# Performance work log

Hardware: AMD Instinct MI355X
Metric: run time of the kernel (lower is better)

## Reference

```python
import jax, jax.numpy as jnp
import numpy as np

N0, N1, N2 = 100000, 25000, 6250
F = 128
OUT = 5


def _mean_agg(feat_src, src, dst, n_dst):
    # DGL copy_u + mean: segment mean over destination nodes (0 for isolated dst)
    s = jax.ops.segment_sum(feat_src[src], dst, num_segments=n_dst)
    cnt = jax.ops.segment_sum(jnp.ones_like(dst, dtype=feat_src.dtype), dst, num_segments=n_dst)
    return s / jnp.maximum(cnt, 1.0)[:, None]


def _graph_conv(feat, src, dst, W, b, n):
    # DGL GraphConv, norm='both': D_src^-1/2 gather-sum D_dst^-1/2, then linear
    dt = feat.dtype
    out_deg = jax.ops.segment_sum(jnp.ones_like(src, dtype=dt), src, num_segments=n)
    in_deg = jax.ops.segment_sum(jnp.ones_like(dst, dtype=dt), dst, num_segments=n)
    ns = jnp.where(out_deg > 0, out_deg ** -0.5, 0.0)
    nd = jnp.where(in_deg > 0, in_deg ** -0.5, 0.0)
    agg = jax.ops.segment_sum((feat * ns[:, None])[src], dst, num_segments=n)
    return (agg * nd[:, None]) @ W + b


def setup_inputs() -> dict:
    key = jax.random.key(0)
    keys = jax.random.split(key, 64)
    _c = iter(range(64))
    def nrm(shape, s=0.05):
        return jax.random.normal(keys[next(_c)], shape, dtype=jnp.float32) * s
    def ri(n, hi):
        return jax.random.randint(keys[next(_c)], (n,), 0, hi)
    inp = {
        'X': nrm((N0, 32), 1.0),
        'g0_src': ri(1600000, N0), 'g0_dst': ri(1600000, N0),
        'g1_src': ri(400000, N1), 'g1_dst': ri(400000, N1),
        'g2_src': ri(100000, N2), 'g2_dst': ri(100000, N2),
        'inc0_src': ri(100000, N0), 'inc0_dst': ri(100000, N1),
        'inc1_src': ri(25000, N1), 'inc1_dst': ri(25000, N2),
        'dec0_src': ri(100000, N2), 'dec0_dst': ri(100000, N1),
        'dec1_src': ri(400000, N1), 'dec1_dst': ri(400000, N0),
        'W_emb': nrm((32, F)), 'b_emb': jnp.zeros((F,), jnp.float32),
        'W_gcn0': nrm((F, F)), 'b_gcn0': jnp.zeros((F,), jnp.float32),
        'W_gcn1': nrm((F, F)), 'b_gcn1': jnp.zeros((F,), jnp.float32),
        'W_gcn2': nrm((F, F)), 'b_gcn2': jnp.zeros((F,), jnp.float32),
        'W_enc0': nrm((F, F)), 'b_enc0': jnp.zeros((F,), jnp.float32),
        'W_enc1': nrm((F, F)), 'b_enc1': jnp.zeros((F,), jnp.float32),
        'W_dec0': nrm((F, F)), 'b_dec0': jnp.zeros((F,), jnp.float32),
        'W_dec1': nrm((F, F)), 'b_dec1': jnp.zeros((F,), jnp.float32),
        'W_head0': nrm((2 * F, OUT)), 'b_head0': jnp.zeros((OUT,), jnp.float32),
        'W_head1': nrm((2 * F, OUT)), 'b_head1': jnp.zeros((OUT,), jnp.float32),
        'W_head2': nrm((2 * F, OUT)), 'b_head2': jnp.zeros((OUT,), jnp.float32),
    }
    return inp


def reference(X, g0_src, g0_dst, g1_src, g1_dst, g2_src, g2_dst,
              inc0_src, inc0_dst, inc1_src, inc1_dst,
              dec0_src, dec0_dst, dec1_src, dec1_dst,
              W_emb, b_emb, W_gcn0, b_gcn0, W_gcn1, b_gcn1, W_gcn2, b_gcn2,
              W_enc0, b_enc0, W_enc1, b_enc1, W_dec0, b_dec0, W_dec1, b_dec1,
              W_head0, b_head0, W_head1, b_head1, W_head2, b_head2):
    # embedding at finest scale
    h0 = X @ W_emb + b_emb                                   # [N0, F]
    # encode + pool fine -> coarse (copy_u/mean)
    h1 = _mean_agg(h0 @ W_enc0 + b_enc0, inc0_src, inc0_dst, N1)   # [N1, F]
    h2 = _mean_agg(h1 @ W_enc1 + b_enc1, inc1_src, inc1_dst, N2)   # [N2, F]
    # intra-scale GraphConv
    g0 = _graph_conv(h0, g0_src, g0_dst, W_gcn0, b_gcn0, N0)
    g1 = _graph_conv(h1, g1_src, g1_dst, W_gcn1, b_gcn1, N1)
    g2 = _graph_conv(h2, g2_src, g2_dst, W_gcn2, b_gcn2, N2)
    # decode coarse -> fine
    d2 = g2
    d1 = _mean_agg(d2 @ W_dec0 + b_dec0, dec0_src, dec0_dst, N1)   # [N1, F]
    d0 = _mean_agg(d1 @ W_dec1 + b_dec1, dec1_src, dec1_dst, N0)   # [N0, F]
    # per-scale heads with softmax
    o0 = jax.nn.softmax(jnp.concatenate([g0, d0], -1) @ W_head0 + b_head0, axis=-1)
    o1 = jax.nn.softmax(jnp.concatenate([g1, d1], -1) @ W_head1 + b_head1, axis=-1)
    o2 = jax.nn.softmax(jnp.concatenate([g2, d2], -1) @ W_head2 + b_head2, axis=-1)
    return jnp.concatenate([o0, o1, o2], axis=0)             # [N0+N1+N2, OUT]
```

## Files before the change

### kernel.cpp

```cpp
#include <hip/hip_runtime.h>

#define F 128
static const int N0 = 100000, N1 = 25000, N2 = 6250;

typedef unsigned short u16;
typedef unsigned int   u32;
typedef __attribute__((ext_vector_type(8))) short bf16x8;
typedef __attribute__((ext_vector_type(4))) float f32x4;

__device__ __forceinline__ float bf2f(u16 u) {
    union { u32 i; float f; } v; v.i = ((u32)u) << 16; return v.f;
}
__device__ __forceinline__ u16 f2bf(float f) {
    u32 u = __float_as_uint(f);
    u += 0x7fff + ((u >> 16) & 1);
    return (u16)(u >> 16);
}

struct Seg7 {
    const int* src[7];
    const int* dst[7];
    int end[7];
    int cbase[7];
    int obase[7];
};

#define EPT 4
#define SM32  (64*(32+8)*2 + 128*(32+8)*2 + 128*4)
#define SM128 (64*(128+8)*2 + 128*(128+8)*2 + 128*4)


template <int K, bool AF32, bool MASK>
__device__ __forceinline__ void dev_mm(char* smem, const void* __restrict__ Ap,
                                       const float* __restrict__ W,
                                       const float* __restrict__ bias,
                                       u16* __restrict__ out,
                                       const int* __restrict__ rowptr,
                                       int M, int blk) {
    const int AST = K + 8;
    const int WST = K + 8;
    u16* Al = (u16*)smem;
    u16* Wt = (u16*)(smem + 64 * AST * 2);
    float* bl = (float*)(smem + 64 * AST * 2 + 128 * WST * 2);
    int tid = threadIdx.x;
    int m0 = blk * 64;

    for (int i = tid; i < K * 128; i += 256) {
        int k = i >> 7, n = i & 127;
        Wt[n * WST + k] = f2bf(W[i]);
    }
    for (int i = tid; i < 64 * K; i += 256) {
        int r = i / K, c = i % K;
        int gr = m0 + r;
        u16 v = 0;
        if (gr < M) {
            if (AF32) v = f2bf(((const float*)Ap)[(size_t)gr * K + c]);
            else      v = ((const u16*)Ap)[(size_t)gr * K + c];
        }
        Al[r * AST + c] = v;
    }
    if (tid < 128) bl[tid] = bias[tid];
    __syncthreads();

    int w = tid >> 6;
    int lane = tid & 63;
    int m16 = lane & 15;
    int quad = lane >> 4;

    f32x4 acc[8];
#pragma unroll
    for (int t = 0; t < 8; t++)
#pragma unroll
        for (int r = 0; r < 4; r++) acc[t][r] = 0.f;

    for (int k0 = 0; k0 < K; k0 += 32) {
        bf16x8 af = *(const bf16x8*)&Al[(w * 16 + m16) * AST + k0 + quad * 8];
#pragma unroll
        for (int t = 0; t < 8; t++) {
            bf16x8 bf = *(const bf16x8*)&Wt[(t * 16 + m16) * WST + k0 + quad * 8];
            acc[t] = __builtin_amdgcn_mfma_f32_16x16x32_bf16(af, bf, acc[t], 0, 0, 0);
        }
    }

#pragma unroll
    for (int t = 0; t < 8; t++) {
#pragma unroll
        for (int r = 0; r < 4; r++) {
            int gr = m0 + w * 16 + quad * 4 + r;
            if (gr >= M) continue;
            int gc = t * 16 + m16;
            bool zrow = false;
            if (MASK) zrow = (rowptr[gr + 1] == rowptr[gr]);
            float v = acc[t][r] + bl[gc];
            out[(size_t)gr * F + gc] = zrow ? (u16)0 : f2bf(v);
        }
    }
}

template <int MODE>
__device__ __forceinline__ void dev_gather(const u16* __restrict__ feat,
                                           const int* __restrict__ rowptr,
                                           const int* __restrict__ col,
                                           const float* __restrict__ odr,
                                           u16* __restrict__ out, int M, int blk) {
    int wv = (blk * 256 + (int)threadIdx.x) >> 6;
    if (wv >= M) return;
    int lane = threadIdx.x & 63;
    int fo = lane << 1;
    int beg = rowptr[wv], end = rowptr[wv + 1];
    float a0 = 0.f, a1 = 0.f;
    int j = beg;
    for (; j + 8 <= end; j += 8) {
        int cc[8];
#pragma unroll
        for (int t = 0; t < 8; t++) cc[t] = col[j + t];
        float ss[8];
#pragma unroll
        for (int t = 0; t < 8; t++) ss[t] = (MODE == 1) ? odr[cc[t]] : 1.f;
        ushort2 uu[8];
#pragma unroll
        for (int t = 0; t < 8; t++) uu[t] = *(const ushort2*)&feat[(size_t)cc[t] * F + fo];
#pragma unroll
        for (int t = 0; t < 8; t++) { a0 += bf2f(uu[t].x) * ss[t]; a1 += bf2f(uu[t].y) * ss[t]; }
    }
    for (; j < end; j++) {
        int c = col[j];
        float s = (MODE == 1) ? odr[c] : 1.f;
        ushort2 u = *(const ushort2*)&feat[(size_t)c * F + fo];
        a0 += bf2f(u.x) * s; a1 += bf2f(u.y) * s;
    }
    int deg = end - beg;
    float fs = (MODE == 0) ? (deg > 0 ? 1.f / (float)deg : 0.f)
                           : (deg > 0 ? rsqrtf((float)deg) : 0.f);
    ushort2 o; o.x = f2bf(a0 * fs); o.y = f2bf(a1 * fs);
    *(ushort2*)&out[(size_t)wv * F + fo] = o;
}

__device__ __forceinline__ void dev_head(char* smem, const u16* __restrict__ g,
                                         const u16* __restrict__ d,
                                         const float* __restrict__ Wh,
                                         const float* __restrict__ bh,
                                         float* __restrict__ out, int M, int blk) {
    float* Wl = (float*)smem;
    float* bl = (float*)(smem + 1280 * 4);
    int tid = threadIdx.x;
    for (int i = tid; i < 1280; i += 256) Wl[i] = Wh[i];
    if (tid < 5) bl[tid] = bh[tid];
    __syncthreads();

    int lane = tid & 63;
    int wv = tid >> 6;
    int r0 = blk * 32 + wv * 8;
    int k0 = lane << 1;
    for (int i = 0; i < 8; i++) {
        int row = r0 + i;
        if (row < M) {
            ushort2 gu = *(const ushort2*)&g[(size_t)row * F + k0];
            ushort2 du = *(const ushort2*)&d[(size_t)row * F + k0];
            float g0v = bf2f(gu.x), g1v = bf2f(gu.y);
            float d0v = bf2f(du.x), d1v = bf2f(du.y);
            float p[5];
#pragma unroll
            for (int o = 0; o < 5; o++) {
                p[o] = g0v * Wl[k0 * 5 + o] + g1v * Wl[(k0 + 1) * 5 + o] +
                       d0v * Wl[(k0 + 128) * 5 + o] + d1v * Wl[(k0 + 129) * 5 + o];
            }
#pragma unroll
            for (int o = 0; o < 5; o++) {
                float v = p[o];
                v += __shfl_xor(v, 32, 64);
                v += __shfl_xor(v, 16, 64);
                v += __shfl_xor(v, 8, 64);
                v += __shfl_xor(v, 4, 64);
                v += __shfl_xor(v, 2, 64);
                v += __shfl_xor(v, 1, 64);
                p[o] = v + bl[o];
            }
            if (lane == 0) {
                float m = p[0];
#pragma unroll
                for (int o = 1; o < 5; o++) m = fmaxf(m, p[o]);
                float e[5], s = 0.f;
#pragma unroll
                for (int o = 0; o < 5; o++) { e[o] = expf(p[o] - m); s += e[o]; }
                float inv = 1.f / s;
#pragma unroll
                for (int o = 0; o < 5; o++) out[(size_t)row * 5 + o] = e[o] * inv;
            }
        }
    }
}


__global__ __launch_bounds__(256) void k_count_emb(Seg7 S, int* __restrict__ cnt,
                                                   int* __restrict__ od,
                                                   u16* __restrict__ occ, int ETOT,
                                                   const float* __restrict__ X,
                                                   const float* __restrict__ Wemb,
                                                   const float* __restrict__ bemb,
                                                   u16* __restrict__ h0, int nbMM) {
    __shared__ char smem[SM32];
    if ((int)blockIdx.x < nbMM) {
        dev_mm<32, true, false>(smem, X, Wemb, bemb, h0, nullptr, N0, blockIdx.x);
        return;
    }
    int e = ((int)blockIdx.x - nbMM) * 256 + threadIdx.x;
    if (e >= ETOT) return;
    int s = 0;
    while (e >= S.end[s]) s++;
    int le = e - ((s == 0) ? 0 : S.end[s - 1]);
    occ[e] = (u16)atomicAdd(&cnt[S.cbase[s] + S.dst[s][le]], 1);
    int ob = S.obase[s];
    if (ob >= 0) atomicAdd(&od[ob + S.src[s][le]], 1);
}

__global__ __launch_bounds__(256) void k_fill_odr(Seg7 S,
                                                  const int* __restrict__ rowptr,
                                                  const u16* __restrict__ occ,
                                                  int* __restrict__ col, int ETOT,
                                                  float invRow, int nbFill,
                                                  const int* __restrict__ od,
                                                  float* __restrict__ odr, int nod) {
    if ((int)blockIdx.x >= nbFill) {
        int i = ((int)blockIdx.x - nbFill) * 256 + threadIdx.x;
        if (i < nod) { int o = od[i]; odr[i] = o > 0 ? rsqrtf((float)o) : 0.f; }
        return;
    }
    int win = blockIdx.x & 7;
    int base = ((int)blockIdx.x >> 3) * (256 * EPT) + threadIdx.x;
#pragma unroll
    for (int t = 0; t < EPT; t++) {
        int e = base + t * 256;
        if (e >= ETOT) break;
        int s = 0;
        while (e >= S.end[s]) s++;
        int le = e - ((s == 0) ? 0 : S.end[s - 1]);
        int grow = S.cbase[s] + S.dst[s][le];
        int w1 = (int)((float)grow * invRow); w1 = w1 > 7 ? 7 : w1;
        if (w1 == win) {
            col[rowptr[grow] + (int)occ[e]] = S.src[s][le];
        }
    }
}

#define SCHUNK 4096
__global__ __launch_bounds__(1024) void k_scan1(const int* __restrict__ cnt,
                                                int* __restrict__ partial, int n) {
    __shared__ int red[1024];
    int tid = threadIdx.x;
    int base = blockIdx.x * SCHUNK + tid * 4;
    int s = 0;
#pragma unroll
    for (int j = 0; j < 4; j++) { int i = base + j; if (i < n) s += cnt[i]; }
    red[tid] = s;
    __syncthreads();
    for (int d = 512; d > 0; d >>= 1) {
        if (tid < d) red[tid] += red[tid + d];
        __syncthreads();
    }
    if (tid == 0) partial[blockIdx.x] = red[0];
}

__global__ __launch_bounds__(128) void k_scan2(int* __restrict__ partial, int G) {
    __shared__ int sh[128];
    int tid = threadIdx.x;
    sh[tid] = (tid < G) ? partial[tid] : 0;
    __syncthreads();
    for (int d = 1; d < 128; d <<= 1) {
        int t = (tid >= d) ? sh[tid - d] : 0;
        __syncthreads();
        sh[tid] += t;
        __syncthreads();
    }
    if (tid < G) partial[tid] = (tid > 0) ? sh[tid - 1] : 0;
    if (tid == 127) partial[G] = sh[127];
}

__global__ __launch_bounds__(1024) void k_scan3(const int* __restrict__ cnt,
                                                const int* __restrict__ partial,
                                                int* __restrict__ rowptr,
                                                int n, int G) {
    __shared__ int red[1024];
    int tid = threadIdx.x;
    int base = blockIdx.x * SCHUNK + tid * 4;
    int v0 = 0, v1 = 0, v2 = 0, v3 = 0;
    if (base + 0 < n) v0 = cnt[base + 0];
    if (base + 1 < n) v1 = cnt[base + 1];
    if (base + 2 < n) v2 = cnt[base + 2];
    if (base + 3 < n) v3 = cnt[base + 3];
    red[tid] = v0 + v1 + v2 + v3;
    __syncthreads();
    for (int d = 1; d < 1024; d <<= 1) {
        int t = (tid >= d) ? red[tid - d] : 0;
        __syncthreads();
        red[tid] += t;
        __syncthreads();
    }
    int off = partial[blockIdx.x] + ((tid > 0) ? red[tid - 1] : 0);
    if (base + 0 < n) { rowptr[base + 0] = off; off += v0; }
    if (base + 1 < n) { rowptr[base + 1] = off; off += v1; }
    if (base + 2 < n) { rowptr[base + 2] = off; off += v2; }
    if (base + 3 < n) { rowptr[base + 3] = off; off += v3; }
    if (blockIdx.x == 0 && tid == 0) rowptr[n] = partial[G];
}

template <int MODE>
__global__ __launch_bounds__(256) void k_gather(const u16* __restrict__ feat,
                                                const int* __restrict__ rowptr,
                                                const int* __restrict__ col,
                                                const float* __restrict__ odr,
                                                u16* __restrict__ out, int M) {
    dev_gather<MODE>(feat, rowptr, col, odr, out, M, blockIdx.x);
}

template <int K, bool AF32, bool MASK>
__global__ __launch_bounds__(256) void k_mm(const void* __restrict__ Ap,
                                            const float* __restrict__ W,
                                            const float* __restrict__ bias,
                                            u16* __restrict__ out,
                                            const int* __restrict__ rowptr,
                                            int M) {
    __shared__ char smem[K == 32 ? SM32 : SM128];
    dev_mm<K, AF32, MASK>(smem, Ap, W, bias, out, rowptr, M, blockIdx.x);
}

template <int MA, int MB>
__global__ __launch_bounds__(256) void k_gather2(
    const u16* fA, const int* rpA, const float* oA, u16* outA, int MAr, int nbA,
    const u16* fB, const int* rpB, const float* oB, u16* outB, int MBr,
    const int* __restrict__ col) {
    if ((int)blockIdx.x < nbA) dev_gather<MA>(fA, rpA, col, oA, outA, MAr, blockIdx.x);
    else                       dev_gather<MB>(fB, rpB, col, oB, outB, MBr, blockIdx.x - nbA);
}

__global__ __launch_bounds__(256) void k_mm2(
    const u16* A1, const float* W1, const float* b1, u16* o1, const int* rp1, int M1, int nb1,
    const u16* A2, const float* W2, const float* b2, u16* o2, int M2) {
    __shared__ char smem[SM128];
    if ((int)blockIdx.x < nb1) dev_mm<128, false, true >(smem, A1, W1, b1, o1, rp1, M1, blockIdx.x);
    else                       dev_mm<128, false, false>(smem, A2, W2, b2, o2, nullptr, M2, blockIdx.x - nb1);
}

__global__ __launch_bounds__(256) void k_head3(
    const u16* Ga, const u16* Da, const float* Wa, const float* Ba, int nb0,
    const u16* Gb, const u16* Db, const float* Wb, const float* Bb, int nb1,
    const u16* Gc, const float* Wc, const float* Bc,
    float* __restrict__ out) {
    __shared__ char smem[1280 * 4 + 32];
    int b = blockIdx.x;
    if (b < nb0)            dev_head(smem, Ga, Da, Wa, Ba, out, N0, b);
    else if (b < nb0 + nb1) dev_head(smem, Gb, Db, Wb, Bb, out + (size_t)N0 * 5, N1, b - nb0);
    else                    dev_head(smem, Gc, Gc, Wc, Bc, out + (size_t)(N0 + N1) * 5, N2, b - nb0 - nb1);
}

extern "C" void kernel_launch(void* const* d_in, const int* in_sizes, int n_in,
                              void* d_out, int out_size, void* d_ws, size_t ws_size,
                              hipStream_t stream) {
    const float* X = (const float*)d_in[0];
    const int *g0s = (const int*)d_in[1], *g0d = (const int*)d_in[2];
    const int *g1s = (const int*)d_in[3], *g1d = (const int*)d_in[4];
    const int *g2s = (const int*)d_in[5], *g2d = (const int*)d_in[6];
    const int *i0s = (const int*)d_in[7], *i0d = (const int*)d_in[8];
    const int *i1s = (const int*)d_in[9], *i1d = (const int*)d_in[10];
    const int *dc0s = (const int*)d_in[11], *dc0d = (const int*)d_in[12];
    const int *dc1s = (const int*)d_in[13], *dc1d = (const int*)d_in[14];
    const float *Wemb = (const float*)d_in[15], *bemb = (const float*)d_in[16];
    const float *Wg0 = (const float*)d_in[17], *bg0 = (const float*)d_in[18];
    const float *Wg1 = (const float*)d_in[19], *bg1 = (const float*)d_in[20];
    const float *Wg2 = (const float*)d_in[21], *bg2 = (const float*)d_in[22];
    const float *We0 = (const float*)d_in[23], *be0 = (const float*)d_in[24];
    const float *We1 = (const float*)d_in[25], *be1 = (const float*)d_in[26];
    const float *Wd0 = (const float*)d_in[27], *bd0 = (const float*)d_in[28];
    const float *Wd1 = (const float*)d_in[29], *bd1 = (const float*)d_in[30];
    const float *Wh0 = (const float*)d_in[31], *bh0 = (const float*)d_in[32];
    const float *Wh1 = (const float*)d_in[33], *bh1 = (const float*)d_in[34];
    const float *Wh2 = (const float*)d_in[35], *bh2 = (const float*)d_in[36];
    const int Eg0 = in_sizes[1], Eg1 = in_sizes[3], Eg2 = in_sizes[5];
    const int Ei0 = in_sizes[7], Ei1 = in_sizes[9];
    const int Ed0 = in_sizes[11], Ed1 = in_sizes[13];
    (void)n_in; (void)out_size; (void)ws_size;

    const int B_I0 = 0;
    const int B_I1 = B_I0 + N1;
    const int B_G2 = B_I1 + N2;
    const int B_D0 = B_G2 + N2;
    const int B_G1 = B_D0 + N1;
    const int B_G0 = B_G1 + N1;
    const int B_D1 = B_G0 + N0;
    const int NROWS = B_D1 + N0;
    const int ETOT  = Eg0 + Eg1 + Eg2 + Ei0 + Ei1 + Ed0 + Ed1;
    const int OB_G0 = 0, OB_G1 = N0, OB_G2 = N0 + N1;
    const int NOD = N0 + N1 + N2;
    const int G = (NROWS + SCHUNK - 1) / SCHUNK;
    const int rowsPerWin = (NROWS + 7) / 8;
    const float invRow = 1.0f / (float)rowsPerWin;
    const int NCH = (ETOT + 256 * EPT - 1) / (256 * EPT);

    char* wsb = (char*)d_ws;
    size_t off = 0;
    auto alloc = [&](size_t bytes) -> char* {
        char* p = wsb + off;
        off = (off + bytes + 255) & ~(size_t)255;
        return p;
    };
    u16* h0  = (u16*)alloc((size_t)N0 * F * 2);
    u16* h1  = (u16*)alloc((size_t)N1 * F * 2);
    u16* h2  = (u16*)alloc((size_t)N2 * F * 2);
    u16* G0  = (u16*)alloc((size_t)N0 * F * 2);
    u16* G1  = (u16*)alloc((size_t)N1 * F * 2);
    u16* G2  = (u16*)alloc((size_t)N2 * F * 2);
    u16* D1  = (u16*)alloc((size_t)N1 * F * 2);
    u16* agg = (u16*)alloc((size_t)N0 * F * 2);
    u16* bN1 = (u16*)alloc((size_t)N1 * F * 2);
    u16* bN2 = (u16*)alloc((size_t)N2 * F * 2);
    u16* pA  = D1;
    u16* D0  = agg;
    int* cnt    = (int*)alloc((size_t)NROWS * 4);
    int* od     = (int*)alloc((size_t)NOD * 4);
    int* rowptr = (int*)alloc((size_t)(NROWS + 1) * 4);
    u16* occ    = (u16*)alloc((size_t)ETOT * 2);
    float* odr  = (float*)alloc((size_t)NOD * 4);
    int* col    = (int*)alloc((size_t)ETOT * 4);
    int* part   = (int*)alloc((size_t)(G + 1) * 4);
    float* out = (float*)d_out;

    Seg7 S;
    S.src[0] = i0s;  S.dst[0] = i0d;  S.cbase[0] = B_I0; S.obase[0] = -1;
    S.src[1] = i1s;  S.dst[1] = i1d;  S.cbase[1] = B_I1; S.obase[1] = -1;
    S.src[2] = g2s;  S.dst[2] = g2d;  S.cbase[2] = B_G2; S.obase[2] = OB_G2;
    S.src[3] = dc0s; S.dst[3] = dc0d; S.cbase[3] = B_D0; S.obase[3] = -1;
    S.src[4] = g1s;  S.dst[4] = g1d;  S.cbase[4] = B_G1; S.obase[4] = OB_G1;
    S.src[5] = g0s;  S.dst[5] = g0d;  S.cbase[5] = B_G0; S.obase[5] = OB_G0;
    S.src[6] = dc1s; S.dst[6] = dc1d; S.cbase[6] = B_D1; S.obase[6] = -1;
    {
        int Es[7] = {Ei0, Ei1, Eg2, Ed0, Eg1, Eg0, Ed1};
        int acc = 0;
        for (int i = 0; i < 7; i++) { acc += Es[i]; S.end[i] = acc; }
    }

    const int nbEmb   = (N0 + 63) / 64;
    const int nbCount = (ETOT + 255) / 256;
    const int nbFill  = NCH * 8;
    const int nbOdr   = (NOD + 255) / 256;

    hipMemsetAsync(cnt, 0, (size_t)((char*)od - (char*)cnt) + (size_t)NOD * 4, stream);
    k_count_emb<<<nbEmb + nbCount, 256, 0, stream>>>(S, cnt, od, occ, ETOT, X, Wemb, bemb, h0, nbEmb);
    k_scan1<<<G, 1024, 0, stream>>>(cnt, part, NROWS);
    k_scan2<<<1, 128, 0, stream>>>(part, G);
    k_scan3<<<G, 1024, 0, stream>>>(cnt, part, rowptr, NROWS, G);
    k_fill_odr<<<nbFill + nbOdr, 256, 0, stream>>>(S, rowptr, occ, col, ETOT, invRow, nbFill, od, odr, NOD);

    {
        int nbA = (N1 + 3) / 4, nbB = (N0 + 3) / 4;
        k_gather2<0, 1><<<nbA + nbB, 256, 0, stream>>>(
            h0, rowptr + B_I0, nullptr, pA, N1, nbA,
            h0, rowptr + B_G0, odr + OB_G0, agg, N0, col);
    }
    {
        int nb1 = (N1 + 63) / 64;
        int nb2 = (N0 + 63) / 64;
        k_mm2<<<nb1 + nb2, 256, 0, stream>>>(pA, We0, be0, h1, rowptr + B_I0, N1, nb1,
                                             agg, Wg0, bg0, G0, N0);
    }
    {
        int nbA = (N2 + 3) / 4, nbB = (N1 + 3) / 4;
        k_gather2<0, 1><<<nbA + nbB, 256, 0, stream>>>(
            h1, rowptr + B_I1, nullptr, bN2, N2, nbA,
            h1, rowptr + B_G1, odr + OB_G1, bN1, N1, col);
    }
    {
        int nb1 = (N2 + 63) / 64;
        int nb2 = (N1 + 63) / 64;
        k_mm2<<<nb1 + nb2, 256, 0, stream>>>(bN2, We1, be1, h2, rowptr + B_I1, N2, nb1,
                                             bN1, Wg1, bg1, G1, N1);
    }
    k_gather<1><<<(N2 + 3) / 4, 256, 0, stream>>>(h2, rowptr + B_G2, col, odr + OB_G2, bN2, N2);
    k_mm<128, false, false><<<(N2 + 63) / 64, 256, 0, stream>>>(bN2, Wg2, bg2, G2, nullptr, N2);
    k_mm<128, false, false><<<(N2 + 63) / 64, 256, 0, stream>>>(G2, Wd0, bd0, bN2, nullptr, N2);
    k_gather<0><<<(N1 + 3) / 4, 256, 0, stream>>>(bN2, rowptr + B_D0, col, nullptr, D1, N1);
    k_mm<128, false, false><<<(N1 + 63) / 64, 256, 0, stream>>>(D1, Wd1, bd1, bN1, nullptr, N1);
    k_gather<0><<<(N0 + 3) / 4, 256, 0, stream>>>(bN1, rowptr + B_D1, col, nullptr, D0, N0);
    {
        int nb0 = (N0 + 31) / 32, nb1 = (N1 + 31) / 32, nb2 = (N2 + 31) / 32;
        k_head3<<<nb0 + nb1 + nb2, 256, 0, stream>>>(G0, D0, Wh0, bh0, nb0,
                                                     G1, D1, Wh1, bh1, nb1,
                                                     G2, Wh2, bh2, out);
    }
}
```

Baseline: 811.7 us.

## Fuse final decode mean-gather into head kernel and batch count atomics per thread

The last decode gather (dec1 mean aggregation into the N0 rows) is now done inside the head kernel for scale 0, so D0 is never written to or read back from global memory and one launch goes away. Separately, the edge-count kernel now handles four edges per thread and issues their atomics back to back, which cuts the block count and lets more atomics be in flight at once. The fused head does the gather in fp32 without rounding D0 to bf16, which changes numerics slightly. The head blocks also become heavier, with less parallelism per row.

```diff
diff --git a/kernel.cpp b/kernel.cpp
--- a/kernel.cpp
+++ b/kernel.cpp
@@ -26,6 +26,7 @@
 };
 
 #define EPT 4
+#define CEPT 4
 #define SM32  (64*(32+8)*2 + 128*(32+8)*2 + 128*4)
 #define SM128 (64*(128+8)*2 + 128*(128+8)*2 + 128*4)
 
@@ -136,8 +137,11 @@
     *(ushort2*)&out[(size_t)wv * F + fo] = o;
 }
 
+template <bool GD>
 __device__ __forceinline__ void dev_head(char* smem, const u16* __restrict__ g,
                                          const u16* __restrict__ d,
+                                         const int* __restrict__ rowptr,
+                                         const int* __restrict__ col,
                                          const float* __restrict__ Wh,
                                          const float* __restrict__ bh,
                                          float* __restrict__ out, int M, int blk) {
@@ -155,10 +159,34 @@
     for (int i = 0; i < 8; i++) {
         int row = r0 + i;
         if (row < M) {
+            float d0v, d1v;
+            if (GD) {
+                int beg = rowptr[row], end = rowptr[row + 1];
+                d0v = 0.f; d1v = 0.f;
+                int j = beg;
+                for (; j + 4 <= end; j += 4) {
+                    int c0 = col[j], c1 = col[j + 1], c2 = col[j + 2], c3 = col[j + 3];
+                    ushort2 u0 = *(const ushort2*)&d[(size_t)c0 * F + k0];
+                    ushort2 u1 = *(const ushort2*)&d[(size_t)c1 * F + k0];
+                    ushort2 u2 = *(const ushort2*)&d[(size_t)c2 * F + k0];
+                    ushort2 u3 = *(const ushort2*)&d[(size_t)c3 * F + k0];
+                    d0v += bf2f(u0.x) + bf2f(u1.x) + bf2f(u2.x) + bf2f(u3.x);
+                    d1v += bf2f(u0.y) + bf2f(u1.y) + bf2f(u2.y) + bf2f(u3.y);
+                }
+                for (; j < end; j++) {
+                    int c = col[j];
+                    ushort2 u = *(const ushort2*)&d[(size_t)c * F + k0];
+                    d0v += bf2f(u.x); d1v += bf2f(u.y);
+                }
+                int deg = end - beg;
+                float fs = deg > 0 ? 1.f / (float)deg : 0.f;
+                d0v *= fs; d1v *= fs;
+            } else {
+                ushort2 du = *(const ushort2*)&d[(size_t)row * F + k0];
+                d0v = bf2f(du.x); d1v = bf2f(du.y);
+            }
             ushort2 gu = *(const ushort2*)&g[(size_t)row * F + k0];
-            ushort2 du = *(const ushort2*)&d[(size_t)row * F + k0];
             float g0v = bf2f(gu.x), g1v = bf2f(gu.y);
-            float d0v = bf2f(du.x), d1v = bf2f(du.y);
             float p[5];
 #pragma unroll
             for (int o = 0; o < 5; o++) {
@@ -204,14 +232,32 @@
         dev_mm<32, true, false>(smem, X, Wemb, bemb, h0, nullptr, N0, blockIdx.x);
         return;
     }
-    int e = ((int)blockIdx.x - nbMM) * 256 + threadIdx.x;
-    if (e >= ETOT) return;
-    int s = 0;
-    while (e >= S.end[s]) s++;
-    int le = e - ((s == 0) ? 0 : S.end[s - 1]);
-    occ[e] = (u16)atomicAdd(&cnt[S.cbase[s] + S.dst[s][le]], 1);
-    int ob = S.obase[s];
-    if (ob >= 0) atomicAdd(&od[ob + S.src[s][le]], 1);
+    int base = ((int)blockIdx.x - nbMM) * (256 * CEPT) + threadIdx.x;
+    int ee[CEPT], grow[CEPT], gs[CEPT];
+#pragma unroll
+    for (int t = 0; t < CEPT; t++) {
+        int e = base + t * 256;
+        ee[t] = e;
+        grow[t] = -1; gs[t] = -1;
+        if (e < ETOT) {
+            int s = 0;
+            while (e >= S.end[s]) s++;
+            int le = e - ((s == 0) ? 0 : S.end[s - 1]);
+            grow[t] = S.cbase[s] + S.dst[s][le];
+            int ob = S.obase[s];
+            if (ob >= 0) gs[t] = ob + S.src[s][le];
+        }
+    }
+    u32 r[CEPT];
+#pragma unroll
+    for (int t = 0; t < CEPT; t++)
+        if (grow[t] >= 0) r[t] = atomicAdd((u32*)&cnt[grow[t]], 1u);
+#pragma unroll
+    for (int t = 0; t < CEPT; t++)
+        if (grow[t] >= 0) occ[ee[t]] = (u16)r[t];
+#pragma unroll
+    for (int t = 0; t < CEPT; t++)
+        if (gs[t] >= 0) atomicAdd(&od[gs[t]], 1);
 }
 
 __global__ __launch_bounds__(256) void k_fill_odr(Seg7 S,
@@ -342,15 +388,16 @@
 }
 
 __global__ __launch_bounds__(256) void k_head3(
-    const u16* Ga, const u16* Da, const float* Wa, const float* Ba, int nb0,
+    const u16* Ga, const u16* dFeat, const int* rpD1, const int* colp,
+    const float* Wa, const float* Ba, int nb0,
     const u16* Gb, const u16* Db, const float* Wb, const float* Bb, int nb1,
     const u16* Gc, const float* Wc, const float* Bc,
     float* __restrict__ out) {
     __shared__ char smem[1280 * 4 + 32];
     int b = blockIdx.x;
-    if (b < nb0)            dev_head(smem, Ga, Da, Wa, Ba, out, N0, b);
-    else if (b < nb0 + nb1) dev_head(smem, Gb, Db, Wb, Bb, out + (size_t)N0 * 5, N1, b - nb0);
-    else                    dev_head(smem, Gc, Gc, Wc, Bc, out + (size_t)(N0 + N1) * 5, N2, b - nb0 - nb1);
+    if (b < nb0)            dev_head<true >(smem, Ga, dFeat, rpD1, colp, Wa, Ba, out, N0, b);
+    else if (b < nb0 + nb1) dev_head<false>(smem, Gb, Db, nullptr, nullptr, Wb, Bb, out + (size_t)N0 * 5, N1, b - nb0);
+    else                    dev_head<false>(smem, Gc, Gc, nullptr, nullptr, Wc, Bc, out + (size_t)(N0 + N1) * 5, N2, b - nb0 - nb1);
 }
 
 extern "C" void kernel_launch(void* const* d_in, const int* in_sizes, int n_in,
@@ -414,7 +461,6 @@
     u16* bN1 = (u16*)alloc((size_t)N1 * F * 2);
     u16* bN2 = (u16*)alloc((size_t)N2 * F * 2);
     u16* pA  = D1;
-    u16* D0  = agg;
     int* cnt    = (int*)alloc((size_t)NROWS * 4);
     int* od     = (int*)alloc((size_t)NOD * 4);
     int* rowptr = (int*)alloc((size_t)(NROWS + 1) * 4);
@@ -439,7 +485,7 @@
     }
 
     const int nbEmb   = (N0 + 63) / 64;
-    const int nbCount = (ETOT + 255) / 256;
+    const int nbCount = (ETOT + 256 * CEPT - 1) / (256 * CEPT);
     const int nbFill  = NCH * 8;
     const int nbOdr   = (NOD + 255) / 256;
 
@@ -479,10 +525,9 @@
     k_mm<128, false, false><<<(N2 + 63) / 64, 256, 0, stream>>>(G2, Wd0, bd0, bN2, nullptr, N2);
     k_gather<0><<<(N1 + 3) / 4, 256, 0, stream>>>(bN2, rowptr + B_D0, col, nullptr, D1, N1);
     k_mm<128, false, false><<<(N1 + 63) / 64, 256, 0, stream>>>(D1, Wd1, bd1, bN1, nullptr, N1);
-    k_gather<0><<<(N0 + 3) / 4, 256, 0, stream>>>(bN1, rowptr + B_D1, col, nullptr, D0, N0);
     {
         int nb0 = (N0 + 31) / 32, nb1 = (N1 + 31) / 32, nb2 = (N2 + 31) / 32;
-        k_head3<<<nb0 + nb1 + nb2, 256, 0, stream>>>(G0, D0, Wh0, bh0, nb0,
+        k_head3<<<nb0 + nb1 + nb2, 256, 0, stream>>>(G0, bN1, rowptr + B_D1, col, Wh0, bh0, nb0,
                                                      G1, D1, Wh1, bh1, nb1,
                                                      G2, Wh2, bh2, out);
     }
```

New measurement: 756.9 us. -6.8%, faster.
